# Kernel tuning notes

Measured on AMD Instinct MI355X. Metric: run time of the kernel, lower is better.

Reference implementation:

```python
import jax, jax.numpy as jnp
import numpy as np

B, L, C = 512, 2048, 32  # batch, seq_len, num_labels


def setup_inputs() -> dict:
    key = jax.random.key(0)
    k1, k2, k3 = jax.random.split(key, 3)
    emissions = jax.random.normal(k1, (B, L, C), dtype=jnp.float32)
    tags = jax.random.randint(k2, (B, L), 0, C, dtype=jnp.int32)
    mask = jnp.ones((B, L), dtype=jnp.int32)
    # learned parameter: transitions (num_labels, num_labels)
    transitions = jax.random.normal(k3, (C, C), dtype=jnp.float32)
    return {"emissions": emissions, "transitions": transitions, "tags": tags, "mask": mask}


def _crf_nll(emissions, transitions, tags, mask):
    Bn, Ln, Cn = emissions.shape
    maskf = mask.astype(emissions.dtype)

    # ---- gold-path score (vectorized over the t loop) ----
    # emit[b,t] = emissions[b,t,tags[b,t]] for t in [0, L-2]
    emit = jnp.take_along_axis(emissions[:, : Ln - 1], tags[:, : Ln - 1, None], axis=2)[..., 0]
    # trans[b,t] = transitions[tags[b,t], tags[b,t+1]]
    trans = transitions[tags[:, : Ln - 1], tags[:, 1:]]
    score = jnp.sum(emit * maskf[:, : Ln - 1] + trans * maskf[:, 1:], axis=1)

    msum = jnp.sum(mask, axis=1)
    last_idx = jnp.clip(msum - 1, 0)  # index of last valid tag
    last_tag = jnp.take_along_axis(tags, last_idx[:, None], axis=1)[:, 0]
    le_t = jnp.clip(msum, 1) - 1
    last_emission = emissions[jnp.arange(Bn), le_t, last_tag]
    score = score + last_emission

    # ---- log-partition via forward algorithm (lax.scan over time) ----
    # Faithful to source: alpha_t[b,n,p] = alpha[b,p] + transitions[n,p] + emit[b,n],
    # reduced over p; the source's mask line is an algebraic no-op (a*m + a*(1-m) = a).
    def step(alpha, emit_t):
        # alpha: (B, C) over prev label p; emit_t: (B, C) over next label n
        alpha_new = jax.nn.logsumexp(alpha[:, None, :] + transitions[None, :, :], axis=2) + emit_t
        return alpha_new, None

    alpha0 = emissions[:, 0]                      # (B, C)
    em_rest = jnp.swapaxes(emissions[:, 1:], 0, 1)  # (L-1, B, C)
    alpha, _ = jax.lax.scan(step, alpha0, em_rest)
    log_Z = jax.nn.logsumexp(alpha, axis=1)       # (B,)

    return jnp.mean(log_Z - score)


def reference(emissions, transitions, tags, mask):
    return _crf_nll(emissions, transitions, tags, mask)
```

## Files before the change

kernel.cpp:

```cpp
#include <hip/hip_runtime.h>
#include <stdint.h>

typedef short bf16x8 __attribute__((ext_vector_type(8)));
typedef float f32x16 __attribute__((ext_vector_type(16)));

#define LOG2E 1.44269504088896340736f
#define LN2f  0.69314718055994530942f

constexpr int Bn = 512;
constexpr int Ln = 2048;
constexpr int Cn = 32;
constexpr int NSEG = 128;
constexpr int SEGLEN = 16;
constexpr int WARM = 8;
constexpr int NGRP = 16;

__device__ __forceinline__ uint32_t pack2_bf16(float lo, float hi) {
    uint32_t a = __float_as_uint(lo) + 0x8000u;
    uint32_t b = __float_as_uint(hi) + 0x8000u;
    return __builtin_amdgcn_perm(b, a, 0x07060302u);
}

__global__ __launch_bounds__(64, 2) void crf_scan(
    const float* __restrict__ emis, const float* __restrict__ trans,
    float* __restrict__ dDelta)
{
    const int lane = threadIdx.x;
    const int h    = lane >> 5;
    const int bl   = lane & 31;
    const int g    = blockIdx.x & (NGRP - 1);
    const int s    = blockIdx.x >> 4;
    const int b    = g * 32 + bl;
    const size_t eb = (size_t)b * Ln * Cn;

    bf16x8 A1, A2;
    {
        float e1[8], e2[8];
        #pragma unroll
        for (int j = 0; j < 8; ++j) {
            int c1 = 4 * h + (j & 3) + 8 * (j >> 2);
            e1[j] = __expf(trans[bl * Cn + c1]);
            e2[j] = __expf(trans[bl * Cn + c1 + 16]);
        }
        union { uint32_t u[4]; bf16x8 v; } ua, ub;
        #pragma unroll
        for (int q = 0; q < 4; ++q) {
            ua.u[q] = pack2_bf16(e1[2*q], e1[2*q+1]);
            ub.u[q] = pack2_bf16(e2[2*q], e2[2*q+1]);
        }
        A1 = ua.v; A2 = ub.v;
    }

    const f32x16 zeroC = {0.f,0.f,0.f,0.f,0.f,0.f,0.f,0.f,0.f,0.f,0.f,0.f,0.f,0.f,0.f,0.f};

    f32x16 Dv;
    bf16x8 B1, B2;
    float offF = 0.f;
    float adj  = 0.f;
    float4 buf[8][4];

    const int t0 = (s == 0) ? 0 : s * SEGLEN - WARM;

    auto loadEm = [&](int t, float4 (&dst)[4]) {
        const float4* p = (const float4*)(emis + eb + (size_t)t * Cn + 4 * h);
        dst[0] = p[0]; dst[1] = p[2]; dst[2] = p[4]; dst[3] = p[6];
    };

    auto packB = [&]() {
        union { uint32_t u[4]; bf16x8 v; } p1, p2;
        #pragma unroll
        for (int q = 0; q < 4; ++q) {
            p1.u[q] = pack2_bf16(Dv[2*q],     Dv[2*q + 1]);
            p2.u[q] = pack2_bf16(Dv[8 + 2*q], Dv[8 + 2*q + 1]);
        }
        B1 = p1.v; B2 = p2.v;
    };

    auto initStep = [&](const float4 (&bu)[4]) {
        #pragma unroll
        for (int q = 0; q < 4; ++q) {
            Dv[4*q+0] = __expf(bu[q].x);
            Dv[4*q+1] = __expf(bu[q].y);
            Dv[4*q+2] = __expf(bu[q].z);
            Dv[4*q+3] = __expf(bu[q].w);
        }
        packB();
    };

    auto stepMfma = [&](const float4 (&bu)[4], float a) {
        f32x16 acc = __builtin_amdgcn_mfma_f32_32x32x16_bf16(A1, B1, zeroC, 0, 0, 0);
        acc = __builtin_amdgcn_mfma_f32_32x32x16_bf16(A2, B2, acc, 0, 0, 0);
        #pragma unroll
        for (int q = 0; q < 4; ++q) {
            float x0 = exp2f(fmaf(bu[q].x, LOG2E, a));
            float x1 = exp2f(fmaf(bu[q].y, LOG2E, a));
            float x2 = exp2f(fmaf(bu[q].z, LOG2E, a));
            float x3 = exp2f(fmaf(bu[q].w, LOG2E, a));
            Dv[4*q+0] = acc[4*q+0] * x0;
            Dv[4*q+1] = acc[4*q+1] * x1;
            Dv[4*q+2] = acc[4*q+2] * x2;
            Dv[4*q+3] = acc[4*q+3] * x3;
        }
        packB();
    };

    auto renorm = [&]() {
        float m0 = fmaxf(fmaxf(Dv[0], Dv[1]),  fmaxf(Dv[2],  Dv[3]));
        float m1 = fmaxf(fmaxf(Dv[4], Dv[5]),  fmaxf(Dv[6],  Dv[7]));
        float m2 = fmaxf(fmaxf(Dv[8], Dv[9]),  fmaxf(Dv[10], Dv[11]));
        float m3 = fmaxf(fmaxf(Dv[12],Dv[13]), fmaxf(Dv[14], Dv[15]));
        float m  = fmaxf(fmaxf(m0, m1), fmaxf(m2, m3));
        m = fmaxf(m, __shfl_xor(m, 32, 64));
        int k = (int)((__float_as_uint(m) >> 23) & 0xffu) - 126;
        offF += (float)k * LN2f;
        adj = -(float)k;
    };

    auto sumD = [&]() {
        float t = 0.f;
        #pragma unroll
        for (int r = 0; r < 16; ++r) t += Dv[r];
        t += __shfl_xor(t, 32, 64);
        return t;
    };

    #pragma unroll
    for (int u = 0; u < 8; ++u) loadEm(t0 + u, buf[u]);

    initStep(buf[0]);
    loadEm(t0 + 8, buf[0]);
    #pragma unroll
    for (int u = 1; u < 8; ++u) {
        stepMfma(buf[u], 0.f);
        loadEm(t0 + 8 + u, buf[u]);
    }

    int nblk;
    if (s == 0) {
        renorm();
        nblk = 1;
    } else {
        float S = sumD();
        adj  = -__log2f(S);
        offF = 0.f;
        nblk = 2;
    }

    #pragma unroll 1
    for (int blk = 0; blk < nblk; ++blk) {
        const bool ld = (blk < nblk - 1);
        #pragma unroll
        for (int u = 0; u < 8; ++u) {
            stepMfma(buf[u], (u == 0) ? adj : 0.f);
            if (ld) loadEm(t0 + 16 + u, buf[u]);
        }
        adj = 0.f;
        if (blk < nblk - 1) renorm();
    }

    float delta = offF + __logf(sumD());
    if (lane < 32) dDelta[s * Bn + b] = delta;
}

__global__ __launch_bounds__(256) void crf_score(
    const float* __restrict__ emis, const float* __restrict__ trans,
    const int* __restrict__ tags, const int* __restrict__ mask,
    float* __restrict__ dScore)
{
    __shared__ float Tl[Cn * Cn];
    __shared__ float sred[4];
    __shared__ int   mred[4];
    const int b   = blockIdx.x;
    const int tid = threadIdx.x;
    for (int i = tid; i < Cn * Cn; i += 256) Tl[i] = trans[i];
    __syncthreads();

    const size_t tB = (size_t)b * Ln;
    const size_t eB = (size_t)b * Ln * Cn;
    float sc = 0.f;
    int   ms = 0;
    #pragma unroll
    for (int k = 0; k < Ln / 256; ++k) {
        int t  = tid + k * 256;
        int tg = tags[tB + t];
        int mk = mask[tB + t];
        ms += mk;
        if (t < Ln - 1) {
            int tg1 = tags[tB + t + 1];
            int mk1 = mask[tB + t + 1];
            sc += (float)mk  * emis[eB + (size_t)t * Cn + tg];
            sc += (float)mk1 * Tl[(tg << 5) + tg1];
        }
    }
    #pragma unroll
    for (int o = 32; o > 0; o >>= 1) {
        sc += __shfl_down(sc, o, 64);
        ms += __shfl_down(ms, o, 64);
    }
    if ((tid & 63) == 0) { sred[tid >> 6] = sc; mred[tid >> 6] = ms; }
    __syncthreads();
    if (tid == 0) {
        float S = 0.f; int M = 0;
        #pragma unroll
        for (int w = 0; w < 4; ++w) { S += sred[w]; M += mred[w]; }
        int last_idx = max(M - 1, 0);
        int le_t     = max(M, 1) - 1;
        int lt = tags[tB + last_idx];
        float le = emis[(tB + le_t) * Cn + lt];
        dScore[b] = S + le;
    }
}

__global__ void crf_final(const float* __restrict__ dDelta,
                          const float* __restrict__ dScore,
                          float* __restrict__ out)
{
    __shared__ float red[8];
    int b = threadIdx.x;
    float lz = 0.f;
    #pragma unroll 8
    for (int s2 = 0; s2 < NSEG; ++s2) lz += dDelta[s2 * Bn + b];
    float val = lz - dScore[b];
    #pragma unroll
    for (int o = 32; o > 0; o >>= 1) val += __shfl_down(val, o, 64);
    if ((b & 63) == 0) red[b >> 6] = val;
    __syncthreads();
    if (b == 0) {
        float t = 0.f;
        #pragma unroll
        for (int w = 0; w < 8; ++w) t += red[w];
        out[0] = t * (1.0f / (float)Bn);
    }
}

extern "C" void kernel_launch(void* const* d_in, const int* in_sizes, int n_in,
                              void* d_out, int out_size, void* d_ws, size_t ws_size,
                              hipStream_t stream)
{
    const float* emis  = (const float*)d_in[0];
    const float* trans = (const float*)d_in[1];
    const int*   tags  = (const int*)d_in[2];
    const int*   mask  = (const int*)d_in[3];
    float* wsf = (float*)d_ws;
    float* dDelta = wsf;
    float* dScore = wsf + NSEG * Bn;
    crf_scan <<<NGRP * NSEG, 64, 0, stream>>>(emis, trans, dDelta);
    crf_score<<<Bn, 256, 0, stream>>>(emis, trans, tags, mask, dScore);
    crf_final<<<1, Bn, 0, stream>>>(dDelta, dScore, (float*)d_out);
}
```

Measured before the change: 232.6 us.

## Shorten scan segments, drop renormalization, and split gold-score kernel across four blocks

The forward scan is split into 256 segments of 8 steps instead of 128 segments of 16, keeping the 8-step warmup. Per-block renormalization is removed and the prefetch buffer shrinks to depth 3, with launch bounds raised to 4 blocks per SIMD to increase occupancy and parallelism. The gold-path score kernel now uses four blocks per batch row writing partial sums, and the last-emission lookup moves into the final reduction kernel. Total warmup work grows relative to useful steps, and dropping renormalization relies on values staying in float range over only 16 steps.

```diff
diff --git a/kernel.cpp b/kernel.cpp
--- a/kernel.cpp
+++ b/kernel.cpp
@@ -5,15 +5,15 @@
 typedef float f32x16 __attribute__((ext_vector_type(16)));
 
 #define LOG2E 1.44269504088896340736f
-#define LN2f  0.69314718055994530942f
 
 constexpr int Bn = 512;
 constexpr int Ln = 2048;
 constexpr int Cn = 32;
-constexpr int NSEG = 128;
-constexpr int SEGLEN = 16;
+constexpr int NSEG = 256;
+constexpr int SEGLEN = 8;
 constexpr int WARM = 8;
 constexpr int NGRP = 16;
+constexpr int DEPTH = 3;
 
 __device__ __forceinline__ uint32_t pack2_bf16(float lo, float hi) {
     uint32_t a = __float_as_uint(lo) + 0x8000u;
@@ -21,7 +21,7 @@
     return __builtin_amdgcn_perm(b, a, 0x07060302u);
 }
 
-__global__ __launch_bounds__(64, 2) void crf_scan(
+__global__ __launch_bounds__(64, 4) void crf_scan(
     const float* __restrict__ emis, const float* __restrict__ trans,
     float* __restrict__ dDelta)
 {
@@ -55,11 +55,11 @@
 
     f32x16 Dv;
     bf16x8 B1, B2;
-    float offF = 0.f;
-    float adj  = 0.f;
-    float4 buf[8][4];
+    float adj = 0.f;
+    float4 buf[DEPTH][4];
 
     const int t0 = (s == 0) ? 0 : s * SEGLEN - WARM;
+    const int nsteps = (s == 0) ? SEGLEN : (WARM + SEGLEN);
 
     auto loadEm = [&](int t, float4 (&dst)[4]) {
         const float4* p = (const float4*)(emis + eb + (size_t)t * Cn + 4 * h);
@@ -104,18 +104,6 @@
         packB();
     };
 
-    auto renorm = [&]() {
-        float m0 = fmaxf(fmaxf(Dv[0], Dv[1]),  fmaxf(Dv[2],  Dv[3]));
-        float m1 = fmaxf(fmaxf(Dv[4], Dv[5]),  fmaxf(Dv[6],  Dv[7]));
-        float m2 = fmaxf(fmaxf(Dv[8], Dv[9]),  fmaxf(Dv[10], Dv[11]));
-        float m3 = fmaxf(fmaxf(Dv[12],Dv[13]), fmaxf(Dv[14], Dv[15]));
-        float m  = fmaxf(fmaxf(m0, m1), fmaxf(m2, m3));
-        m = fmaxf(m, __shfl_xor(m, 32, 64));
-        int k = (int)((__float_as_uint(m) >> 23) & 0xffu) - 126;
-        offF += (float)k * LN2f;
-        adj = -(float)k;
-    };
-
     auto sumD = [&]() {
         float t = 0.f;
         #pragma unroll
@@ -125,52 +113,47 @@
     };
 
     #pragma unroll
-    for (int u = 0; u < 8; ++u) loadEm(t0 + u, buf[u]);
-
-    initStep(buf[0]);
-    loadEm(t0 + 8, buf[0]);
-    #pragma unroll
-    for (int u = 1; u < 8; ++u) {
-        stepMfma(buf[u], 0.f);
-        loadEm(t0 + 8 + u, buf[u]);
-    }
-
-    int nblk;
+    for (int u = 0; u < DEPTH; ++u) loadEm(t0 + u, buf[u]);
+
     if (s == 0) {
-        renorm();
-        nblk = 1;
+        initStep(buf[0]);
+        loadEm(t0 + DEPTH, buf[0]);
+        #pragma unroll
+        for (int u = 1; u < SEGLEN; ++u) {
+            stepMfma(buf[u % DEPTH], 0.f);
+            if (u + DEPTH < SEGLEN) loadEm(t0 + DEPTH + u, buf[u % DEPTH]);
+        }
     } else {
+        initStep(buf[0]);
+        loadEm(t0 + DEPTH, buf[0]);
+        #pragma unroll
+        for (int u = 1; u < WARM; ++u) {
+            stepMfma(buf[u % DEPTH], 0.f);
+            loadEm(t0 + DEPTH + u, buf[u % DEPTH]);
+        }
         float S = sumD();
-        adj  = -__log2f(S);
-        offF = 0.f;
-        nblk = 2;
-    }
-
-    #pragma unroll 1
-    for (int blk = 0; blk < nblk; ++blk) {
-        const bool ld = (blk < nblk - 1);
-        #pragma unroll
-        for (int u = 0; u < 8; ++u) {
-            stepMfma(buf[u], (u == 0) ? adj : 0.f);
-            if (ld) loadEm(t0 + 16 + u, buf[u]);
-        }
-        adj = 0.f;
-        if (blk < nblk - 1) renorm();
-    }
-
-    float delta = offF + __logf(sumD());
+        adj = -__log2f(S);
+        #pragma unroll
+        for (int u = WARM; u < WARM + SEGLEN; ++u) {
+            stepMfma(buf[u % DEPTH], (u == WARM) ? adj : 0.f);
+            if (u + DEPTH < WARM + SEGLEN) loadEm(t0 + DEPTH + u, buf[u % DEPTH]);
+        }
+    }
+
+    float delta = __logf(sumD());
     if (lane < 32) dDelta[s * Bn + b] = delta;
 }
 
 __global__ __launch_bounds__(256) void crf_score(
     const float* __restrict__ emis, const float* __restrict__ trans,
     const int* __restrict__ tags, const int* __restrict__ mask,
-    float* __restrict__ dScore)
+    float* __restrict__ dScoreP, int* __restrict__ dMsumP)
 {
     __shared__ float Tl[Cn * Cn];
     __shared__ float sred[4];
     __shared__ int   mred[4];
-    const int b   = blockIdx.x;
+    const int b   = blockIdx.x >> 2;
+    const int q   = blockIdx.x & 3;
     const int tid = threadIdx.x;
     for (int i = tid; i < Cn * Cn; i += 256) Tl[i] = trans[i];
     __syncthreads();
@@ -180,8 +163,8 @@
     float sc = 0.f;
     int   ms = 0;
     #pragma unroll
-    for (int k = 0; k < Ln / 256; ++k) {
-        int t  = tid + k * 256;
+    for (int k = 0; k < 2; ++k) {
+        int t  = q * 512 + k * 256 + tid;
         int tg = tags[tB + t];
         int mk = mask[tB + t];
         ms += mk;
@@ -203,16 +186,16 @@
         float S = 0.f; int M = 0;
         #pragma unroll
         for (int w = 0; w < 4; ++w) { S += sred[w]; M += mred[w]; }
-        int last_idx = max(M - 1, 0);
-        int le_t     = max(M, 1) - 1;
-        int lt = tags[tB + last_idx];
-        float le = emis[(tB + le_t) * Cn + lt];
-        dScore[b] = S + le;
+        dScoreP[blockIdx.x] = S;
+        dMsumP [blockIdx.x] = M;
     }
 }
 
 __global__ void crf_final(const float* __restrict__ dDelta,
-                          const float* __restrict__ dScore,
+                          const float* __restrict__ dScoreP,
+                          const int* __restrict__ dMsumP,
+                          const int* __restrict__ tags,
+                          const float* __restrict__ emis,
                           float* __restrict__ out)
 {
     __shared__ float red[8];
@@ -220,7 +203,14 @@
     float lz = 0.f;
     #pragma unroll 8
     for (int s2 = 0; s2 < NSEG; ++s2) lz += dDelta[s2 * Bn + b];
-    float val = lz - dScore[b];
+    float sc = 0.f; int ms = 0;
+    #pragma unroll
+    for (int q = 0; q < 4; ++q) { sc += dScoreP[b * 4 + q]; ms += dMsumP[b * 4 + q]; }
+    int last_idx = max(ms - 1, 0);
+    int le_t     = max(ms, 1) - 1;
+    int lt = tags[(size_t)b * Ln + last_idx];
+    float le = emis[((size_t)b * Ln + le_t) * Cn + lt];
+    float val = lz - (sc + le);
     #pragma unroll
     for (int o = 32; o > 0; o >>= 1) val += __shfl_down(val, o, 64);
     if ((b & 63) == 0) red[b >> 6] = val;
@@ -242,9 +232,10 @@
     const int*   tags  = (const int*)d_in[2];
     const int*   mask  = (const int*)d_in[3];
     float* wsf = (float*)d_ws;
-    float* dDelta = wsf;
-    float* dScore = wsf + NSEG * Bn;
+    float* dDelta  = wsf;
+    float* dScoreP = wsf + NSEG * Bn;
+    int*   dMsumP  = (int*)(wsf + NSEG * Bn + 2048);
     crf_scan <<<NGRP * NSEG, 64, 0, stream>>>(emis, trans, dDelta);
-    crf_score<<<Bn, 256, 0, stream>>>(emis, trans, tags, mask, dScore);
-    crf_final<<<1, Bn, 0, stream>>>(dDelta, dScore, (float*)d_out);
-}
+    crf_score<<<4 * Bn, 256, 0, stream>>>(emis, trans, tags, mask, dScoreP, dMsumP);
+    crf_final<<<1, Bn, 0, stream>>>(dDelta, dScoreP, dMsumP, tags, emis, (float*)d_out);
+}
```

New measurement: 249.8 us. 7.4% more time.
